# Kernel tuning notes

Measured on AMD Instinct MI355X. Metric: run time of the kernel, lower is better.

## Reference

```python
import jax, jax.numpy as jnp
import numpy as np
import math

N_EMBD = 2048
N_HEAD = 16
HEAD_DIM = N_EMBD // N_HEAD
B, T = 2, 2048


def setup_inputs() -> dict:
    key = jax.random.key(0)
    k1, k2, k3 = jax.random.split(key, 3)
    x = jax.random.normal(k1, (B, T, N_EMBD), dtype=jnp.float32)
    # Linear weights stored torch-style [out, in]; applied as x @ W.T
    W_gate = jax.random.normal(k2, (N_HEAD, N_EMBD), dtype=jnp.float32) * 0.02
    W_qkv = jax.random.normal(k3, (3 * N_EMBD, N_EMBD), dtype=jnp.float32) * 0.02
    return {"x": x, "W_gate": W_gate, "W_qkv": W_qkv}


def reference(x, W_gate, W_qkv):
    Bb, Tt, C = x.shape
    H, hd = N_HEAD, HEAD_DIM
    # --- top-1 head gating ---
    gating = jax.nn.softmax(x @ W_gate.T, axis=-1)            # [B,T,H]
    idx = jnp.argmax(gating, axis=-1)                          # [B,T]
    indicator = jax.nn.one_hot(idx, H, dtype=gating.dtype)     # [B,T,H] (no grad, like scatter of ones)
    top1_val = jnp.max(gating, axis=-1, keepdims=True)         # [B,T,1]
    gating_top1 = indicator * top1_val                         # [B,T,H]
    # --- qkv projection ---
    qkv = x @ W_qkv.T                                          # [B,T,3C]
    q, k, v = jnp.split(qkv, 3, axis=-1)
    k = k.reshape(Bb, Tt, H, hd)
    v = v.reshape(Bb, Tt, H, hd)
    # scatter-style weighted collapse of heads -> single shared K/V head (MQA)
    k_shared = jnp.einsum('bth,bthd->btd', indicator, k)       # [B,T,hd]
    v_shared = jnp.einsum('bth,bthd->btd', gating_top1, v)     # [B,T,hd]
    q = q.reshape(Bb, Tt, H, hd).transpose(0, 2, 1, 3)         # [B,H,T,hd]
    # --- causal softmax attention (materialized, as in source) ---
    att = jnp.einsum('bhqd,bkd->bhqk', q, k_shared) * (1.0 / math.sqrt(hd))
    causal = jnp.tril(jnp.ones((Tt, Tt), dtype=bool))          # [T,T]
    att = jnp.where(causal[None, None, :, :], att, -jnp.inf)
    att = jax.nn.softmax(att, axis=-1)
    y = jnp.einsum('bhqk,bkd->bhqd', att, v_shared)            # [B,H,T,hd]
    y = y.transpose(0, 2, 1, 3).reshape(Bb, Tt, C)
    return y
```

## Files before the change

### kernel.cpp

```cpp
#include <hip/hip_runtime.h>
#include <math.h>
#include <cstddef>

#define BB 2
#define TT 2048
#define CC 2048
#define HH 16
#define HD 128
#define MM (BB * TT)
#define QKV_N 6144
#define BK 32

typedef __attribute__((ext_vector_type(8))) short short8;
typedef __attribute__((ext_vector_type(4))) float f32x4;

__device__ __forceinline__ unsigned short f2bf(float f) {
    union { float f; unsigned int u; } v; v.f = f;
    unsigned int r = v.u + 0x7FFFu + ((v.u >> 16) & 1u);
    return (unsigned short)(r >> 16);
}
__device__ __forceinline__ unsigned short f2bf_up(float f) {
    union { float f; unsigned int u; } v; v.f = f;
    return (unsigned short)((v.u + 0x8000u) >> 16);
}
__device__ __forceinline__ float bf2f(unsigned short s) {
    union { unsigned int u; float f; } v; v.u = ((unsigned int)s) << 16;
    return v.f;
}
__device__ __forceinline__ void gload16(const void* g, void* l) {
    __builtin_amdgcn_global_load_lds(
        (const __attribute__((address_space(1))) unsigned int*)g,
        (__attribute__((address_space(3))) unsigned int*)l, 16, 0, 0);
}

__global__ __launch_bounds__(256) void gate_kernel(const float* __restrict__ x,
                                                   const float* __restrict__ Wg,
                                                   int* __restrict__ idxbuf,
                                                   float* __restrict__ top1buf,
                                                   unsigned short* __restrict__ xb) {
    int m = blockIdx.x;
    int tid = threadIdx.x;
    int h = tid >> 4;
    int j = tid & 15;
    const float4* xr = (const float4*)(x + (size_t)m * CC);
    const float4* wr = (const float4*)(Wg + (size_t)h * CC);
    float acc = 0.f;
#pragma unroll 8
    for (int i = 0; i < CC / 4; i += 16) {
        float4 a = xr[i + j];
        float4 b = wr[i + j];
        acc += a.x * b.x + a.y * b.y + a.z * b.z + a.w * b.w;
    }
    for (int off = 8; off > 0; off >>= 1) acc += __shfl_down(acc, off, 16);
    __shared__ float logits[HH];
    if (j == 0) logits[h] = acc;
    {
        float4 a = xr[tid * 2], b = xr[tid * 2 + 1];
        union { unsigned short s[8]; uint4 u; } pk;
        pk.s[0] = f2bf(a.x); pk.s[1] = f2bf(a.y); pk.s[2] = f2bf(a.z); pk.s[3] = f2bf(a.w);
        pk.s[4] = f2bf(b.x); pk.s[5] = f2bf(b.y); pk.s[6] = f2bf(b.z); pk.s[7] = f2bf(b.w);
        ((uint4*)(xb + (size_t)m * CC))[tid] = pk.u;
    }
    __syncthreads();
    if (tid == 0) {
        float zmax = logits[0];
        int best = 0;
        for (int i = 1; i < HH; i++) {
            if (logits[i] > zmax) { zmax = logits[i]; best = i; }
        }
        float s = 0.f;
        for (int i = 0; i < HH; i++) s += expf(logits[i] - zmax);
        idxbuf[m] = best;
        top1buf[m] = 1.0f / s;
    }
}

__global__ __launch_bounds__(256) void convert_bf16(const float* __restrict__ src,
                                                    unsigned short* __restrict__ dst,
                                                    int n8) {
    int i = blockIdx.x * 256 + threadIdx.x;
    if (i >= n8) return;
    const float4* s4 = (const float4*)src;
    float4 a = s4[i * 2], b = s4[i * 2 + 1];
    union { unsigned short s[8]; uint4 u; } pk;
    pk.s[0] = f2bf(a.x); pk.s[1] = f2bf(a.y); pk.s[2] = f2bf(a.z); pk.s[3] = f2bf(a.w);
    pk.s[4] = f2bf(b.x); pk.s[5] = f2bf(b.y); pk.s[6] = f2bf(b.z); pk.s[7] = f2bf(b.w);
    ((uint4*)dst)[i] = pk.u;
}

__global__ __launch_bounds__(256) void qproj_gemm(const unsigned short* __restrict__ A,
                                                  const unsigned short* __restrict__ Bm,
                                                  unsigned short* __restrict__ C) {
    __shared__ unsigned short As[128 * BK];
    __shared__ unsigned short Bs[128 * BK];
    int tid = threadIdx.x;
    int wave = tid >> 6, lane = tid & 63;
    int l = lane & 15, g = lane >> 4;
    int flat = blockIdx.y * gridDim.x + blockIdx.x;
    int xcd = flat & 7, pos = flat >> 3;
    flat = xcd * 64 + pos;
    int m0 = (flat >> 4) * 128, n0 = (flat & 15) * 128;
    int wr = wave >> 1, wc = wave & 1;

    f32x4 acc[4][4];
#pragma unroll
    for (int i = 0; i < 4; i++)
#pragma unroll
        for (int j = 0; j < 4; j++) acc[i][j] = (f32x4){0.f, 0.f, 0.f, 0.f};

    int srow = lane >> 2;
    int scol = (lane & 3) * 8;
    const unsigned short* aB0 = A + (size_t)(m0 + wave * 32 + srow) * 2048 + scol;
    const unsigned short* bB0 = Bm + (size_t)(n0 + wave * 32 + srow) * 2048 + scol;
    unsigned short* aL0 = &As[wave * 1024];
    unsigned short* bL0 = &Bs[wave * 1024];

    for (int k0 = 0; k0 < 2048; k0 += BK) {
        __syncthreads();
        gload16(aB0 + k0, aL0);
        gload16(aB0 + k0 + (size_t)16 * 2048, aL0 + 512);
        gload16(bB0 + k0, bL0);
        gload16(bB0 + k0 + (size_t)16 * 2048, bL0 + 512);
        __syncthreads();
        short8 af[4], bf[4];
#pragma unroll
        for (int i = 0; i < 4; i++)
            af[i] = *(const short8*)&As[(wr * 64 + i * 16 + l) * BK + g * 8];
#pragma unroll
        for (int j = 0; j < 4; j++)
            bf[j] = *(const short8*)&Bs[(wc * 64 + j * 16 + l) * BK + g * 8];
#pragma unroll
        for (int i = 0; i < 4; i++)
#pragma unroll
            for (int j = 0; j < 4; j++)
                acc[i][j] = __builtin_amdgcn_mfma_f32_16x16x32_bf16(af[i], bf[j], acc[i][j], 0, 0, 0);
    }

    const float qscale = 0.08838834764831845f;
#pragma unroll
    for (int j = 0; j < 4; j++) {
        int col = n0 + wc * 64 + j * 16 + l;
#pragma unroll
        for (int i = 0; i < 4; i++) {
            int row = m0 + wr * 64 + i * 16 + g * 4;
#pragma unroll
            for (int r = 0; r < 4; r++)
                C[(size_t)(row + r) * CC + col] = f2bf(acc[i][j][r] * qscale);
        }
    }
}

__global__ __launch_bounds__(256) void bucket_kernel(const int* __restrict__ idxb,
                                                     int* __restrict__ ord,
                                                     int* __restrict__ hs) {
    __shared__ unsigned short cnts[256][16];
    __shared__ int hsum[16], hbase[16];
    int t = threadIdx.x;
    unsigned short c[16];
#pragma unroll
    for (int h = 0; h < 16; h++) c[h] = 0;
    int hv[16];
#pragma unroll
    for (int i = 0; i < 16; i++) {
        hv[i] = idxb[t * 16 + i];
        c[hv[i]]++;
    }
#pragma unroll
    for (int h = 0; h < 16; h++) cnts[t][h] = c[h];
    __syncthreads();
    if (t < 16) {
        int s = 0;
        for (int j = 0; j < 256; j++) {
            int v = cnts[j][t];
            cnts[j][t] = (unsigned short)s;
            s += v;
        }
        hsum[t] = s;
    }
    __syncthreads();
    if (t == 0) {
        int s = 0;
        for (int h = 0; h < 16; h++) { hbase[h] = s; hs[h] = s; s += hsum[h]; }
        hs[16] = s;
    }
    __syncthreads();
    int pos[16];
#pragma unroll
    for (int h = 0; h < 16; h++) pos[h] = hbase[h] + (int)cnts[t][h];
#pragma unroll
    for (int i = 0; i < 16; i++) {
        int h = hv[i];
        ord[pos[h]++] = t * 16 + i;
    }
}

__global__ __launch_bounds__(256) void kvsel_gemm(const unsigned short* __restrict__ xb,
                                                  const unsigned short* __restrict__ wb,
                                                  const int* __restrict__ ord,
                                                  const int* __restrict__ hs,
                                                  const float* __restrict__ top1,
                                                  unsigned short* __restrict__ kshB,
                                                  unsigned short* __restrict__ vshT) {
    __shared__ unsigned short As[64 * 32];
    __shared__ unsigned short Bs[128 * 32];
    int h = blockIdx.x, reg = blockIdx.y, mt = blockIdx.z;
    int s0 = hs[h], s1 = hs[h + 1];
    int cnt = s1 - s0;
    if (mt * 64 >= cnt) return;
    int base = s0 + mt * 64;
    int tid = threadIdx.x;
    int wave = tid >> 6, lane = tid & 63;
    int l = lane & 15, g = lane >> 4;

    int arow = base + wave * 16 + (lane >> 2);
    int atok = ord[(arow < s1) ? arow : (s1 - 1)];
    const unsigned short* aSrc = xb + (size_t)atok * CC + (lane & 3) * 8;
    unsigned short* aDst = &As[wave * 512];
    int wr0 = 2048 + reg * 2048 + h * 128;
    const unsigned short* bSrc0 = wb + (size_t)(wr0 + (wave * 2 + 0) * 16 + (lane >> 2)) * CC + (lane & 3) * 8;
    const unsigned short* bSrc1 = wb + (size_t)(wr0 + (wave * 2 + 1) * 16 + (lane >> 2)) * CC + (lane & 3) * 8;
    unsigned short* bDst0 = &Bs[(wave * 2 + 0) * 512];
    unsigned short* bDst1 = &Bs[(wave * 2 + 1) * 512];

    f32x4 acc[8];
#pragma unroll
    for (int j = 0; j < 8; j++) acc[j] = (f32x4){0.f, 0.f, 0.f, 0.f};

    for (int k0 = 0; k0 < 2048; k0 += 32) {
        __syncthreads();
        gload16(aSrc + k0, aDst);
        gload16(bSrc0 + k0, bDst0);
        gload16(bSrc1 + k0, bDst1);
        __syncthreads();
        short8 af = *(const short8*)&As[(wave * 16 + l) * 32 + g * 8];
#pragma unroll
        for (int j = 0; j < 8; j++) {
            short8 bf = *(const short8*)&Bs[(j * 16 + l) * 32 + g * 8];
            acc[j] = __builtin_amdgcn_mfma_f32_16x16x32_bf16(af, bf, acc[j], 0, 0, 0);
        }
    }
#pragma unroll
    for (int i = 0; i < 4; i++) {
        int r = wave * 16 + g * 4 + i;
        if (base + r >= s1) continue;
        int tok = ord[base + r];
        if (reg == 0) {
#pragma unroll
            for (int j = 0; j < 8; j++)
                kshB[(size_t)tok * HD + j * 16 + l] = f2bf(acc[j][i]);
        } else {
            float tv = top1[tok];
#pragma unroll
            for (int j = 0; j < 8; j++)
                vshT[(size_t)(j * 16 + l) * MM + tok] = f2bf(acc[j][i] * tv);
        }
    }
}

__global__ __launch_bounds__(256) void attn_mfma(const unsigned short* __restrict__ qb,
                                                 const unsigned short* __restrict__ kb,
                                                 const unsigned short* __restrict__ vtb,
                                                 float* __restrict__ y) {
    __shared__ unsigned short KsA[2][32 * 128];
    __shared__ unsigned short VtA[2][128 * 32];
    __shared__ unsigned short Ps[4][2][16][40];

    int bid = blockIdx.x;
    int ql = 64 + (bid >> 3);
    int b  = (bid >> 2) & 1;
    int hq = bid & 3;
    int qs = 127 - ql;
    int q0l = ql * 16, q0s = qs * 16;
    int nchL = (ql >> 1) + 1;
    int nchS = (qs >> 1) + 1;
    int tid = threadIdx.x;
    int wave = tid >> 6;
    int lane = tid & 63;
    int l = lane & 15;
    int g = lane >> 4;
    int h = hq * 4 + wave;

    short8 qf[2][4];
#pragma unroll
    for (int qt = 0; qt < 2; qt++) {
        int q0 = qt ? q0s : q0l;
        const unsigned short* qrow = qb + (size_t)(b * TT + q0 + l) * CC + h * HD;
#pragma unroll
        for (int kc = 0; kc < 4; kc++)
            qf[qt][kc] = *(const short8*)(qrow + kc * 32 + g * 8);
    }

    short8 onesf;
    {
        short v = (l == 0) ? (short)0x3F80 : (short)0;
#pragma unroll
        for (int e = 0; e < 8; e++) onesf[e] = v;
    }

    f32x4 o[2][8];
    f32x4 o8[2];
#pragma unroll
    for (int qt = 0; qt < 2; qt++) {
#pragma unroll
        for (int n = 0; n < 8; n++) o[qt][n] = (f32x4){0.f, 0.f, 0.f, 0.f};
        o8[qt] = (f32x4){0.f, 0.f, 0.f, 0.f};
    }

    const unsigned short* kbase = kb + (size_t)b * TT * HD;
    int rbaseL = q0l + g * 4;
    int rbaseS = q0s + g * 4;

#define STAGE(cc, bufi) do {                                                      \
        int kc0_ = (cc) * 32;                                                     \
        _Pragma("unroll")                                                         \
        for (int rep_ = 0; rep_ < 2; rep_++) {                                    \
            int s_ = tid + rep_ * 256;                                            \
            int kr_ = s_ >> 4, kp_ = s_ & 15;                                     \
            gload16(kbase + (size_t)(kc0_ + kr_) * HD + ((kp_ ^ (kr_ & 15)) * 8), \
                    &KsA[bufi][(rep_ * 256 + wave * 64) * 8]);                    \
            int vd_ = s_ >> 2, vp_ = s_ & 3;                                      \
            int vq_ = vp_ ^ ((vd_ >> 1) & 3);                                     \
            gload16(vtb + (size_t)vd_ * MM + b * TT + kc0_ + vq_ * 8,             \
                    &VtA[bufi][(rep_ * 256 + wave * 64) * 8]);                    \
        }                                                                         \
    } while (0)

    STAGE(0, 0);
    __syncthreads();

    for (int c = 0; c < nchL; c++) {
        int kc0 = c * 32;
        int cur = c & 1;
        if (c + 1 < nchL) STAGE(c + 1, cur ^ 1);
        bool sAct = (c < nchS);
        bool diagL = (c == nchL - 1);
        bool diagS = (c == nchS - 1);
        const unsigned short* Kc = KsA[cur];
        const unsigned short* Vc = VtA[cur];

#pragma unroll
        for (int t = 0; t < 2; t++) {
            short8 kf[4];
#pragma unroll
            for (int kc = 0; kc < 4; kc++)
                kf[kc] = *(const short8*)&Kc[(t * 16 + l) * 128 + (((kc * 4 + g) ^ l) * 8)];
            f32x4 sl = (f32x4){0.f, 0.f, 0.f, 0.f};
#pragma unroll
            for (int kc = 0; kc < 4; kc++)
                sl = __builtin_amdgcn_mfma_f32_16x16x32_bf16(qf[0][kc], kf[kc], sl, 0, 0, 0);
            if (diagL) {
                int key = kc0 + t * 16 + l;
#pragma unroll
                for (int i = 0; i < 4; i++)
                    if (key > rbaseL + i) sl[i] = -1e30f;
            }
#pragma unroll
            for (int i = 0; i < 4; i++)
                Ps[wave][0][g * 4 + i][t * 16 + l] = f2bf_up(__expf(sl[i] - 30.f));
            if (sAct) {
                f32x4 ss = (f32x4){0.f, 0.f, 0.f, 0.f};
#pragma unroll
                for (int kc = 0; kc < 4; kc++)
                    ss = __builtin_amdgcn_mfma_f32_16x16x32_bf16(qf[1][kc], kf[kc], ss, 0, 0, 0);
                if (diagS) {
                    int key = kc0 + t * 16 + l;
#pragma unroll
                    for (int i = 0; i < 4; i++)
                        if (key > rbaseS + i) ss[i] = -1e30f;
                }
#pragma unroll
                for (int i = 0; i < 4; i++)
                    Ps[wave][1][g * 4 + i][t * 16 + l] = f2bf_up(__expf(ss[i] - 30.f));
            }
        }
        {
            short8 pf0 = *(const short8*)&Ps[wave][0][l][g * 8];
            if (sAct) {
                short8 pf1 = *(const short8*)&Ps[wave][1][l][g * 8];
#pragma unroll
                for (int n = 0; n < 8; n++) {
                    short8 vf = *(const short8*)&Vc[(n * 16 + l) * 32 + ((g ^ ((l >> 1) & 3)) * 8)];
                    o[0][n] = __builtin_amdgcn_mfma_f32_16x16x32_bf16(pf0, vf, o[0][n], 0, 0, 0);
                    o[1][n] = __builtin_amdgcn_mfma_f32_16x16x32_bf16(pf1, vf, o[1][n], 0, 0, 0);
                }
                o8[0] = __builtin_amdgcn_mfma_f32_16x16x32_bf16(pf0, onesf, o8[0], 0, 0, 0);
                o8[1] = __builtin_amdgcn_mfma_f32_16x16x32_bf16(pf1, onesf, o8[1], 0, 0, 0);
            } else {
#pragma unroll
                for (int n = 0; n < 8; n++) {
                    short8 vf = *(const short8*)&Vc[(n * 16 + l) * 32 + ((g ^ ((l >> 1) & 3)) * 8)];
                    o[0][n] = __builtin_amdgcn_mfma_f32_16x16x32_bf16(pf0, vf, o[0][n], 0, 0, 0);
                }
                o8[0] = __builtin_amdgcn_mfma_f32_16x16x32_bf16(pf0, onesf, o8[0], 0, 0, 0);
            }
        }
        __syncthreads();
    }
#undef STAGE

#pragma unroll
    for (int qt = 0; qt < 2; qt++) {
        int q0 = qt ? q0s : q0l;
        float inv[4];
#pragma unroll
        for (int i = 0; i < 4; i++) {
            float lv = __shfl(o8[qt][i], lane & 48);
            inv[i] = 1.f / lv;
        }
#pragma unroll
        for (int n = 0; n < 8; n++) {
#pragma unroll
            for (int i = 0; i < 4; i++) {
                y[(size_t)(b * TT + q0 + g * 4 + i) * CC + h * HD + n * 16 + l] =
                    o[qt][n][i] * inv[i];
            }
        }
    }
}

extern "C" void kernel_launch(void* const* d_in, const int* in_sizes, int n_in,
                              void* d_out, int out_size, void* d_ws, size_t ws_size,
                              hipStream_t stream) {
    (void)in_sizes; (void)n_in; (void)out_size; (void)ws_size;
    const float* x    = (const float*)d_in[0];
    const float* Wg   = (const float*)d_in[1];
    const float* Wqkv = (const float*)d_in[2];
    float* y = (float*)d_out;

    unsigned short* xb   = (unsigned short*)d_ws;
    unsigned short* wb   = xb + (size_t)MM * CC;
    unsigned short* qbuf = wb + (size_t)QKV_N * CC;
    unsigned short* kshB = qbuf + (size_t)MM * CC;
    unsigned short* vshT = kshB + (size_t)MM * HD;
    float* top1 = (float*)(vshT + (size_t)HD * MM);
    int*   idxb = (int*)(top1 + MM);
    int*   ord  = idxb + MM;
    int*   hs   = ord + MM;

    gate_kernel<<<MM, 256, 0, stream>>>(x, Wg, idxb, top1, xb);
    convert_bf16<<<(QKV_N * CC / 8 + 255) / 256, 256, 0, stream>>>(Wqkv, wb, QKV_N * CC / 8);
    qproj_gemm<<<dim3(16, 32), 256, 0, stream>>>(xb, wb, qbuf);
    bucket_kernel<<<1, 256, 0, stream>>>(idxb, ord, hs);
    kvsel_gemm<<<dim3(16, 2, 64), 256, 0, stream>>>(xb, wb, ord, hs, top1, kshB, vshT);
    attn_mfma<<<512, 256, 0, stream>>>(qbuf, kshB, vshT, y);
}
```

Baseline: 334.3 us.

## Double-buffer LDS tiles in Q-projection and KV-select GEMMs

Both GEMM kernels now use two LDS buffers per operand. The next K-slice's global-to-LDS loads are issued before the MFMAs on the current slice, and there is one barrier per iteration instead of two. This aims to hide global load latency behind compute, at the cost of twice the shared memory, which may lower occupancy. The q-projection also drops its XCD-aware block remapping and uses plain blockIdx tiling, which changes L2 locality.

Result: no change. 333.5 us (-0.2%).

```diff
diff --git a/kernel.cpp b/kernel.cpp
--- a/kernel.cpp
+++ b/kernel.cpp
@@ -91,15 +91,12 @@
 __global__ __launch_bounds__(256) void qproj_gemm(const unsigned short* __restrict__ A,
                                                   const unsigned short* __restrict__ Bm,
                                                   unsigned short* __restrict__ C) {
-    __shared__ unsigned short As[128 * BK];
-    __shared__ unsigned short Bs[128 * BK];
+    __shared__ unsigned short As[2][128 * BK];
+    __shared__ unsigned short Bs[2][128 * BK];
     int tid = threadIdx.x;
     int wave = tid >> 6, lane = tid & 63;
     int l = lane & 15, g = lane >> 4;
-    int flat = blockIdx.y * gridDim.x + blockIdx.x;
-    int xcd = flat & 7, pos = flat >> 3;
-    flat = xcd * 64 + pos;
-    int m0 = (flat >> 4) * 128, n0 = (flat & 15) * 128;
+    int m0 = blockIdx.y * 128, n0 = blockIdx.x * 128;
     int wr = wave >> 1, wc = wave & 1;
 
     f32x4 acc[4][4];
@@ -112,29 +109,35 @@
     int scol = (lane & 3) * 8;
     const unsigned short* aB0 = A + (size_t)(m0 + wave * 32 + srow) * 2048 + scol;
     const unsigned short* bB0 = Bm + (size_t)(n0 + wave * 32 + srow) * 2048 + scol;
-    unsigned short* aL0 = &As[wave * 1024];
-    unsigned short* bL0 = &Bs[wave * 1024];
+
+#define QSTAGE(k0_, bi) do {                                                   \
+        gload16(aB0 + (k0_), &As[bi][wave * 1024]);                            \
+        gload16(aB0 + (k0_) + (size_t)16 * 2048, &As[bi][wave * 1024 + 512]);  \
+        gload16(bB0 + (k0_), &Bs[bi][wave * 1024]);                            \
+        gload16(bB0 + (k0_) + (size_t)16 * 2048, &Bs[bi][wave * 1024 + 512]);  \
+    } while (0)
+
+    QSTAGE(0, 0);
+    __syncthreads();
 
     for (int k0 = 0; k0 < 2048; k0 += BK) {
-        __syncthreads();
-        gload16(aB0 + k0, aL0);
-        gload16(aB0 + k0 + (size_t)16 * 2048, aL0 + 512);
-        gload16(bB0 + k0, bL0);
-        gload16(bB0 + k0 + (size_t)16 * 2048, bL0 + 512);
-        __syncthreads();
+        int cur = (k0 >> 5) & 1;
+        if (k0 + BK < 2048) QSTAGE(k0 + BK, cur ^ 1);
         short8 af[4], bf[4];
 #pragma unroll
         for (int i = 0; i < 4; i++)
-            af[i] = *(const short8*)&As[(wr * 64 + i * 16 + l) * BK + g * 8];
+            af[i] = *(const short8*)&As[cur][(wr * 64 + i * 16 + l) * BK + g * 8];
 #pragma unroll
         for (int j = 0; j < 4; j++)
-            bf[j] = *(const short8*)&Bs[(wc * 64 + j * 16 + l) * BK + g * 8];
+            bf[j] = *(const short8*)&Bs[cur][(wc * 64 + j * 16 + l) * BK + g * 8];
 #pragma unroll
         for (int i = 0; i < 4; i++)
 #pragma unroll
             for (int j = 0; j < 4; j++)
                 acc[i][j] = __builtin_amdgcn_mfma_f32_16x16x32_bf16(af[i], bf[j], acc[i][j], 0, 0, 0);
-    }
+        __syncthreads();
+    }
+#undef QSTAGE
 
     const float qscale = 0.08838834764831845f;
 #pragma unroll
@@ -201,8 +204,8 @@
                                                   const float* __restrict__ top1,
                                                   unsigned short* __restrict__ kshB,
                                                   unsigned short* __restrict__ vshT) {
-    __shared__ unsigned short As[64 * 32];
-    __shared__ unsigned short Bs[128 * 32];
+    __shared__ unsigned short As[2][64 * 32];
+    __shared__ unsigned short Bs[2][128 * 32];
     int h = blockIdx.x, reg = blockIdx.y, mt = blockIdx.z;
     int s0 = hs[h], s1 = hs[h + 1];
     int cnt = s1 - s0;
@@ -215,30 +218,36 @@
     int arow = base + wave * 16 + (lane >> 2);
     int atok = ord[(arow < s1) ? arow : (s1 - 1)];
     const unsigned short* aSrc = xb + (size_t)atok * CC + (lane & 3) * 8;
-    unsigned short* aDst = &As[wave * 512];
     int wr0 = 2048 + reg * 2048 + h * 128;
     const unsigned short* bSrc0 = wb + (size_t)(wr0 + (wave * 2 + 0) * 16 + (lane >> 2)) * CC + (lane & 3) * 8;
     const unsigned short* bSrc1 = wb + (size_t)(wr0 + (wave * 2 + 1) * 16 + (lane >> 2)) * CC + (lane & 3) * 8;
-    unsigned short* bDst0 = &Bs[(wave * 2 + 0) * 512];
-    unsigned short* bDst1 = &Bs[(wave * 2 + 1) * 512];
+
+#define KSTAGE(k0_, bi) do {                                    \
+        gload16(aSrc + (k0_), &As[bi][wave * 512]);             \
+        gload16(bSrc0 + (k0_), &Bs[bi][(wave * 2 + 0) * 512]);  \
+        gload16(bSrc1 + (k0_), &Bs[bi][(wave * 2 + 1) * 512]);  \
+    } while (0)
 
     f32x4 acc[8];
 #pragma unroll
     for (int j = 0; j < 8; j++) acc[j] = (f32x4){0.f, 0.f, 0.f, 0.f};
 
+    KSTAGE(0, 0);
+    __syncthreads();
+
     for (int k0 = 0; k0 < 2048; k0 += 32) {
+        int cur = (k0 >> 5) & 1;
+        if (k0 + 32 < 2048) KSTAGE(k0 + 32, cur ^ 1);
+        short8 af = *(const short8*)&As[cur][(wave * 16 + l) * 32 + g * 8];
+#pragma unroll
+        for (int j = 0; j < 8; j++) {
+            short8 bf = *(const short8*)&Bs[cur][(j * 16 + l) * 32 + g * 8];
+            acc[j] = __builtin_amdgcn_mfma_f32_16x16x32_bf16(af, bf, acc[j], 0, 0, 0);
+        }
         __syncthreads();
-        gload16(aSrc + k0, aDst);
-        gload16(bSrc0 + k0, bDst0);
-        gload16(bSrc1 + k0, bDst1);
-        __syncthreads();
-        short8 af = *(const short8*)&As[(wave * 16 + l) * 32 + g * 8];
-#pragma unroll
-        for (int j = 0; j < 8; j++) {
-            short8 bf = *(const short8*)&Bs[(j * 16 + l) * 32 + g * 8];
-            acc[j] = __builtin_amdgcn_mfma_f32_16x16x32_bf16(af, bf, acc[j], 0, 0, 0);
-        }
-    }
+    }
+#undef KSTAGE
+
 #pragma unroll
     for (int i = 0; i < 4; i++) {
         int r = wave * 16 + g * 4 + i;
```
